# Optimization experiments

Measured on AMD Instinct MI355X. Metric: run time of the kernel, lower is better.

The kernel has to match this reference:

```python
import jax, jax.numpy as jnp
import numpy as np

B, N, K, NUM_CLASSES = 8, 4096, 20, 40


def _knn_idx(x, k):
    # x: [B, N, D] -> indices of k nearest neighbors (self excluded), [B, N, k]
    sq = jnp.sum(x * x, axis=-1)  # [B, N]
    dist = sq[:, :, None] + sq[:, None, :] - 2.0 * jnp.einsum('bnd,bmd->bnm', x, x)
    dist = jnp.where(jnp.eye(x.shape[1], dtype=bool)[None], jnp.inf, dist)
    return jax.lax.top_k(-dist, k)[1]


def _edge_conv(x, idx, params):
    # PyG EdgeConv with max aggregation: max_j MLP([x_i, x_j - x_i])
    x_j = jax.vmap(lambda xb, ib: xb[ib])(x, idx)              # [B, N, K, D]
    x_i = jnp.broadcast_to(x[:, :, None, :], x_j.shape)        # [B, N, K, D]
    h = jnp.concatenate([x_i, x_j - x_i], axis=-1)             # [B, N, K, 2D]
    for w, b in params:
        h = jax.nn.relu(h @ w + b)
    return jnp.max(h, axis=2)                                  # [B, N, out]


def setup_inputs() -> dict:
    key = jax.random.key(0)
    ks = jax.random.split(key, 12)

    def lin(k, i, o):  # torch Linear default init
        k1, k2 = jax.random.split(k)
        s = 1.0 / np.sqrt(i)
        return (jax.random.uniform(k1, (i, o), jnp.float32, -s, s),
                jax.random.uniform(k2, (o,), jnp.float32, -s, s))

    inp = {
        'pos': jax.random.normal(ks[0], (B * N, 3), jnp.float32),
        'batch': jnp.repeat(jnp.arange(B, dtype=jnp.int32), N),
    }
    names = [('m1w1', 'm1b1', 6, 64), ('m1w2', 'm1b2', 64, 64), ('m1w3', 'm1b3', 64, 64),
             ('m2w1', 'm2b1', 128, 128), ('m2w2', 'm2b2', 128, 128), ('m2w3', 'm2b3', 128, 256),
             ('lin0_w', 'lin0_b', 256, 512), ('lin1_w', 'lin1_b', 512, 256),
             ('lin2_w', 'lin2_b', 256, 256), ('lin3_w', 'lin3_b', 256, NUM_CLASSES)]
    for t, (wn, bn, i, o) in enumerate(names):
        w, b = lin(ks[t + 1], i, o)
        inp[wn] = w
        inp[bn] = b
    return inp


def reference(pos, batch, m1w1, m1b1, m1w2, m1b2, m1w3, m1b3,
              m2w1, m2b1, m2w2, m2b2, m2w3, m2b3,
              lin0_w, lin0_b, lin1_w, lin1_b, lin2_w, lin2_b, lin3_w, lin3_b):
    x = pos.reshape(B, N, 3)
    x = _edge_conv(x, _knn_idx(x, K), [(m1w1, m1b1), (m1w2, m1b2), (m1w3, m1b3)])   # [B,N,64]
    x = _edge_conv(x, _knn_idx(x, K), [(m2w1, m2b1), (m2w2, m2b2), (m2w3, m2b3)])   # [B,N,256]
    x = jax.nn.relu(x @ lin0_w + lin0_b)                                            # [B,N,512]
    x = jax.ops.segment_max(x.reshape(B * N, -1), batch, num_segments=B)            # [B,512]
    x = jax.nn.relu(x @ lin1_w + lin1_b)
    x = jax.nn.relu(x @ lin2_w + lin2_b)   # dropout is identity in eval mode
    x = x @ lin3_w + lin3_b
    return jax.nn.log_softmax(x, axis=-1)
```

## Files before the change

### kernel.cpp

```cpp
#include <hip/hip_runtime.h>

#define DEVI static __device__ __forceinline__

typedef __attribute__((ext_vector_type(4))) float f32x4;
typedef __attribute__((ext_vector_type(8))) short short8;
typedef __attribute__((ext_vector_type(4))) short short4v;
typedef __attribute__((ext_vector_type(8))) __bf16 bf16x8;

#define N_    4096
#define KNN_  20
#define NPTS  32768

DEVI unsigned short f2bf(float f){
  unsigned u = __float_as_uint(f);
  u += 0x7FFFu + ((u >> 16) & 1u);
  return (unsigned short)(u >> 16);
}
DEVI float bf2f(unsigned short s){ return __uint_as_float(((unsigned)s) << 16); }
DEVI float bf2fs(short s){ return __uint_as_float(((unsigned)(unsigned short)s) << 16); }
DEVI unsigned umin32(unsigned a, unsigned b){ return a < b ? a : b; }
DEVI unsigned umax32(unsigned a, unsigned b){ return a > b ? a : b; }

DEVI f32x4 mfma16(short8 a, short8 b, f32x4 c){
  return __builtin_amdgcn_mfma_f32_16x16x32_bf16(
      __builtin_bit_cast(bf16x8, a), __builtin_bit_cast(bf16x8, b), c, 0, 0, 0);
}

DEVI short8 lds_frag(const unsigned short* buf, int row, int k0, int strideS, int swzMask){
  return *(const short8*)(buf + row*strideS + (k0 ^ ((row & swzMask) << 3)));
}
DEVI void lds_put8(unsigned short* buf, int row, int k0, int strideS, int swzMask, short8 v){
  *(short8*)(buf + row*strideS + (k0 ^ ((row & swzMask) << 3))) = v;
}
DEVI void lds_put1(unsigned short* buf, int row, int col, int strideS, int swzMask, unsigned short v){
  buf[row*strideS + (col ^ ((row & swzMask) << 3))] = v;
}

DEVI void ins32(unsigned K, unsigned (&a)[20]){
#pragma unroll
  for (int t = 19; t >= 1; --t) a[t] = umin32(a[t], umax32(a[t-1], K));
  a[0] = umin32(a[0], K);
}
DEVI void ins64(double K, double (&a)[20]){
#pragma unroll
  for (int t = 19; t >= 1; --t) a[t] = fmin(a[t], fmax(a[t-1], K));
  a[0] = fmin(a[0], K);
}

__global__ __launch_bounds__(256) void p3_k(const float* __restrict__ pos,
    unsigned short* __restrict__ p3h, unsigned short* __restrict__ p3l, float* __restrict__ nrm3){
  int p = blockIdx.x*256 + threadIdx.x;
  if (p >= NPTS) return;
  float x = pos[(size_t)p*3], y = pos[(size_t)p*3+1], z = pos[(size_t)p*3+2];
  float v[8] = {x, y, z, 0.f, 0.f, 0.f, 0.f, 0.f};
#pragma unroll
  for (int c = 0; c < 8; ++c){
    unsigned short h = f2bf(v[c]);
    p3h[(size_t)p*8 + c] = h;
    p3l[(size_t)p*8 + c] = f2bf(v[c] - bf2f(h));
  }
  nrm3[p] = fmaf(x, x, fmaf(y, y, z*z));
}

template<int MODE>
__global__ __launch_bounds__(256) void knn_k(const unsigned short* __restrict__ Xh,
                                             const unsigned short* __restrict__ Xl,
                                             const float* __restrict__ nrm,
                                             unsigned* __restrict__ pk){
  constexpr int OBL  = MODE ? 8192  : 1024;
  constexpr int OS   = MODE ? 16384 : 2048;
  constexpr int OBUF = MODE ? 33536 : 19200;
  constexpr int OSQ  = MODE ? 39680 : 25344;
  __shared__ __align__(16) char smem[MODE ? 39936 : 25600];
  unsigned short* Bh = (unsigned short*)(smem);
  unsigned short* Bl = (unsigned short*)(smem + OBL);
  unsigned* S        = (unsigned*)(smem + OS);
  unsigned* buf      = (unsigned*)(smem + OBUF);
  float* sqj         = (float*)(smem + OSQ);
  unsigned* mD       = (unsigned*)(smem);

  const int blk = blockIdx.x;
  const int rt = blk & 63, ch = (blk >> 6) & 1, bb = blk >> 7;
  const int rowbase = rt * 64, cbase = ch * 2048;
  const size_t gb = (size_t)bb * N_;
  const int tid = threadIdx.x, lane = tid & 63, wid = tid >> 6;
  const int l15 = lane & 15, kL = (lane >> 4) << 3, r0 = (lane >> 4) << 2;

  short8 ah0 = {0,0,0,0,0,0,0,0}, ah1 = {0,0,0,0,0,0,0,0};
  short8 al0 = {0,0,0,0,0,0,0,0}, al1 = {0,0,0,0,0,0,0,0};
  const int arow = rowbase + (wid << 4) + l15;
  if (MODE == 1){
    const size_t ab = (gb + arow) * 64;
    ah0 = *(const short8*)(Xh + ab + kL);
    ah1 = *(const short8*)(Xh + ab + 32 + kL);
    al0 = *(const short8*)(Xl + ab + kL);
    al1 = *(const short8*)(Xl + ab + 32 + kL);
  } else {
    if (lane < 16){
      const size_t ab = (gb + arow) * 8;
      ah0 = *(const short8*)(Xh + ab);
      al0 = *(const short8*)(Xl + ab);
    }
  }
  float sqi[4];
#pragma unroll
  for (int r = 0; r < 4; ++r) sqi[r] = nrm[gb + rowbase + (wid << 4) + r0 + r];

  unsigned arr[20];
#pragma unroll
  for (int t = 0; t < 20; ++t) arr[t] = 0xFFFFFFFFu;
  unsigned thrP = 0xFFFFFFFFu;
  int cnt = 0;
  const int srow = tid & 63, q = tid >> 6;

  for (int c = 0; c < 32; ++c){
    __syncthreads();
    if (MODE == 1){
      for (int f = tid; f < 512; f += 256){
        int lf = f & 63, half = (f >> 6) & 1, nt = f >> 7;
        int row = nt*16 + (lf & 15);
        int col = half*32 + ((lf >> 4) << 3);
        const size_t src = (gb + cbase + c*64 + row) * 64 + col;
        *(short8*)(Bh + f*8) = *(const short8*)(Xh + src);
        *(short8*)(Bl + f*8) = *(const short8*)(Xl + src);
      }
    } else {
      if (tid < 64)       *(short8*)(Bh + tid*8)      = *(const short8*)(Xh + (gb + cbase + c*64 + tid)*8);
      else if (tid < 128) *(short8*)(Bl + (tid-64)*8) = *(const short8*)(Xl + (gb + cbase + c*64 + (tid-64))*8);
    }
    if (tid < 64) sqj[tid] = nrm[gb + cbase + c*64 + tid];
    __syncthreads();

    const bool selfTile = (cbase + c*64 == rowbase);
#pragma unroll
    for (int nt = 0; nt < 4; ++nt){
      f32x4 acc = {0.f,0.f,0.f,0.f};
      if (MODE == 1){
        const int fb = lane*8;
        short8 bh0 = *(const short8*)(Bh + (nt*2+0)*512 + fb);
        short8 bh1 = *(const short8*)(Bh + (nt*2+1)*512 + fb);
        short8 bl0 = *(const short8*)(Bl + (nt*2+0)*512 + fb);
        short8 bl1 = *(const short8*)(Bl + (nt*2+1)*512 + fb);
        acc = mfma16(ah0, bh0, acc); acc = mfma16(ah1, bh1, acc);
        acc = mfma16(ah0, bl0, acc); acc = mfma16(ah1, bl1, acc);
        acc = mfma16(al0, bh0, acc); acc = mfma16(al1, bh1, acc);
      } else {
        int br = nt*16 + l15;
        short8 bh = {0,0,0,0,0,0,0,0}, bl = {0,0,0,0,0,0,0,0};
        if (lane < 16){
          bh = *(const short8*)(Bh + br*8);
          bl = *(const short8*)(Bl + br*8);
        }
        acc = mfma16(ah0, bh, acc);
        acc = mfma16(ah0, bl, acc);
        acc = mfma16(al0, bh, acc);
      }
      int col = nt*16 + l15;
      float sj = sqj[col];
      unsigned cid = (unsigned)(c*64 + col);
#pragma unroll
      for (int r = 0; r < 4; ++r){
        int row = (wid << 4) + r0 + r;
        float dv = fmaxf(fmaf(-2.f, acc[r], sqi[r] + sj), 0.f);
        unsigned kb = (__float_as_uint(dv) & ~0x7FFu) | cid;
        if (selfTile && col == row) kb = 0x7F800000u | cid;
        S[row*67 + col] = kb;
      }
    }
    __syncthreads();

    {
      const unsigned* Sr = S + srow*67 + q*16;
#pragma unroll
      for (int u = 0; u < 16; ++u){
        unsigned kb = Sr[u];
        if (kb < thrP){
          if (cnt < 6){ buf[cnt*256 + tid] = kb; ++cnt; }
          else ins32(kb, arr);
        }
      }
      for (int t = 0; t < cnt; ++t) ins32(buf[t*256 + tid], arr);
      cnt = 0;
      thrP = arr[19];
    }
  }
  __syncthreads();
  if (q > 0){
#pragma unroll
    for (int t = 0; t < 20; ++t) mD[(srow*3 + q-1)*20 + t] = arr[t];
  }
  __syncthreads();
  if (q == 0){
    for (int qq = 0; qq < 3; ++qq)
#pragma unroll
      for (int t = 0; t < 20; ++t) ins32(mD[(srow*3 + qq)*20 + t], arr);
    const size_t gp = gb + rowbase + srow;
#pragma unroll
    for (int t = 0; t < 20; ++t) pk[((size_t)(ch*20 + t))*NPTS + gp] = arr[t];
  }
}

__global__ __launch_bounds__(256) void knn_merge_k(const unsigned* __restrict__ pk,
                                                   int* __restrict__ idx){
  const int p = blockIdx.x*256 + threadIdx.x;
  double arr[20];
#pragma unroll
  for (int t = 0; t < 20; ++t){
    unsigned k = pk[(size_t)t*NPTS + p];
    unsigned long long K = (((unsigned long long)(k & ~0x7FFu)) << 1) | (k & 0x7FFu);
    arr[t] = __builtin_bit_cast(double, K);
  }
#pragma unroll
  for (int t = 0; t < 20; ++t){
    unsigned k = pk[(size_t)(20 + t)*NPTS + p];
    unsigned long long K = (((unsigned long long)(k & ~0x7FFu)) << 1) | (2048u + (k & 0x7FFu));
    ins64(__builtin_bit_cast(double, K), arr);
  }
  int* o = idx + (size_t)p*KNN_;
#pragma unroll
  for (int t = 0; t < 20; ++t)
    o[t] = (int)(__builtin_bit_cast(unsigned long long, arr[t]) & 0xFFFu);
}

__global__ void stage_w_k(const float* __restrict__ src, unsigned short* __restrict__ dh,
                          unsigned short* __restrict__ dl, int K, int Nw, int KT, int NT){
  int tid = blockIdx.x*256 + threadIdx.x;
  if (tid >= NT*KT*64) return;
  int l = tid & 63;
  int kk = (tid >> 6) % KT;
  int nt = tid / (64*KT);
  int n = nt*16 + (l & 15);
  int kb = kk*32 + ((l >> 4) << 3);
#pragma unroll
  for (int e=0;e<8;++e){
    int k = kb + e;
    float w = (k < K) ? src[(size_t)k*Nw + n] : 0.f;
    unsigned short h = f2bf(w);
    dh[(size_t)tid*8 + e] = h;
    if (dl) dl[(size_t)tid*8 + e] = f2bf(w - bf2f(h));
  }
}

__global__ __launch_bounds__(256) void ec1_k(const float* __restrict__ pos, const int* __restrict__ idx1,
    const unsigned short* __restrict__ W1h, const unsigned short* __restrict__ W1l,
    const unsigned short* __restrict__ W2h, const unsigned short* __restrict__ W2l,
    const unsigned short* __restrict__ W3h, const unsigned short* __restrict__ W3l,
    const float* __restrict__ b1, const float* __restrict__ b2, const float* __restrict__ b3,
    unsigned short* __restrict__ x1h, unsigned short* __restrict__ x1l, float* __restrict__ nrm1){
  __shared__ __align__(16) char smem[52224];
  unsigned short* Ah  = (unsigned short*)(smem);
  unsigned short* Al  = (unsigned short*)(smem + 5120);
  unsigned short* H1h = (unsigned short*)(smem + 10240);
  unsigned short* H1l = (unsigned short*)(smem + 20480);
  unsigned short* H2h = (unsigned short*)(smem + 30720);
  unsigned short* H2l = (unsigned short*)(smem + 40960);
  unsigned* pmax = (unsigned*)(smem + 51200);
  const int p0 = blockIdx.x * 4;
  const int bb = p0 >> 12;
  const int tid = threadIdx.x, lane = tid & 63, wid = tid >> 6;
  pmax[tid] = 0u;
  if (tid < 80){
    int p = p0 + tid/20, slot = tid%20;
    int j = idx1[(size_t)p*KNN_ + slot];
    int gj = (bb << 12) + j;
    float a6[6];
    a6[0] = pos[(size_t)p*3]; a6[1] = pos[(size_t)p*3+1]; a6[2] = pos[(size_t)p*3+2];
    a6[3] = pos[(size_t)gj*3]   - a6[0];
    a6[4] = pos[(size_t)gj*3+1] - a6[1];
    a6[5] = pos[(size_t)gj*3+2] - a6[2];
#pragma unroll
    for (int q=0;q<4;++q){
      short8 vh, vl;
#pragma unroll
      for (int c=0;c<8;++c){
        int cc = q*8+c;
        float v = 0.f;
        if (cc < 6) v = a6[cc];
        unsigned short h = f2bf(v);
        vh[c] = (short)h;
        vl[c] = (short)f2bf(v - bf2f(h));
      }
      lds_put8(Ah, tid, q*8, 32, 3, vh);
      lds_put8(Al, tid, q*8, 32, 3, vl);
    }
  }
  __syncthreads();
  const int l15 = lane & 15, kL = (lane >> 4) << 3, r0 = (lane >> 4) << 2;
  {
    int nt = wid;
    short8 wh = *(const short8*)(W1h + ((size_t)nt*64 + lane)*8);
    short8 wl = *(const short8*)(W1l + ((size_t)nt*64 + lane)*8);
    float bias = b1[nt*16 + l15];
    for (int mt=0; mt<5; ++mt){
      int ar = mt*16 + l15;
      short8 ah = lds_frag(Ah, ar, kL, 32, 3);
      short8 al = lds_frag(Al, ar, kL, 32, 3);
      f32x4 acc = {0.f,0.f,0.f,0.f};
      acc = mfma16(ah, wh, acc);
      acc = mfma16(ah, wl, acc);
      acc = mfma16(al, wh, acc);
#pragma unroll
      for (int r=0;r<4;++r){
        int row = mt*16 + r0 + r;
        float v = fmaxf(acc[r] + bias, 0.f);
        unsigned short h = f2bf(v);
        lds_put1(H1h, row, nt*16+l15, 64, 7, h);
        lds_put1(H1l, row, nt*16+l15, 64, 7, f2bf(v - bf2f(h)));
      }
    }
  }
  __syncthreads();
  {
    int nt = wid;
    short8 wh0 = *(const short8*)(W2h + ((size_t)(nt*2+0)*64 + lane)*8);
    short8 wh1 = *(const short8*)(W2h + ((size_t)(nt*2+1)*64 + lane)*8);
    short8 wl0 = *(const short8*)(W2l + ((size_t)(nt*2+0)*64 + lane)*8);
    short8 wl1 = *(const short8*)(W2l + ((size_t)(nt*2+1)*64 + lane)*8);
    float bias = b2[nt*16 + l15];
    for (int mt=0; mt<5; ++mt){
      int ar = mt*16 + l15;
      short8 ah0 = lds_frag(H1h, ar, kL,      64, 7);
      short8 ah1 = lds_frag(H1h, ar, 32 + kL, 64, 7);
      short8 al0 = lds_frag(H1l, ar, kL,      64, 7);
      short8 al1 = lds_frag(H1l, ar, 32 + kL, 64, 7);
      f32x4 acc = {0.f,0.f,0.f,0.f};
      acc = mfma16(ah0, wh0, acc); acc = mfma16(ah1, wh1, acc);
      acc = mfma16(ah0, wl0, acc); acc = mfma16(ah1, wl1, acc);
      acc = mfma16(al0, wh0, acc); acc = mfma16(al1, wh1, acc);
#pragma unroll
      for (int r=0;r<4;++r){
        int row = mt*16 + r0 + r;
        float v = fmaxf(acc[r] + bias, 0.f);
        unsigned short h = f2bf(v);
        lds_put1(H2h, row, nt*16+l15, 64, 7, h);
        lds_put1(H2l, row, nt*16+l15, 64, 7, f2bf(v - bf2f(h)));
      }
    }
  }
  __syncthreads();
  {
    int nt = wid;
    short8 wh0 = *(const short8*)(W3h + ((size_t)(nt*2+0)*64 + lane)*8);
    short8 wh1 = *(const short8*)(W3h + ((size_t)(nt*2+1)*64 + lane)*8);
    short8 wl0 = *(const short8*)(W3l + ((size_t)(nt*2+0)*64 + lane)*8);
    short8 wl1 = *(const short8*)(W3l + ((size_t)(nt*2+1)*64 + lane)*8);
    float bias = b3[nt*16 + l15];
    for (int mt=0; mt<5; ++mt){
      int ar = mt*16 + l15;
      short8 ah0 = lds_frag(H2h, ar, kL,      64, 7);
      short8 ah1 = lds_frag(H2h, ar, 32 + kL, 64, 7);
      short8 al0 = lds_frag(H2l, ar, kL,      64, 7);
      short8 al1 = lds_frag(H2l, ar, 32 + kL, 64, 7);
      f32x4 acc = {0.f,0.f,0.f,0.f};
      acc = mfma16(ah0, wh0, acc); acc = mfma16(ah1, wh1, acc);
      acc = mfma16(ah0, wl0, acc); acc = mfma16(ah1, wl1, acc);
      acc = mfma16(al0, wh0, acc); acc = mfma16(al1, wh1, acc);
#pragma unroll
      for (int r=0;r<4;++r){
        int row = mt*16 + r0 + r;
        float v = fmaxf(acc[r] + bias, 0.f);
        atomicMax(&pmax[(row/20)*64 + nt*16 + l15], __float_as_uint(v));
      }
    }
  }
  __syncthreads();
  if (tid < 128){
    int p = tid >> 5, cp = tid & 31;
    int c0 = cp*2, c1 = c0 + 1;
    float m0 = __uint_as_float(pmax[p*64 + c0]);
    float m1 = __uint_as_float(pmax[p*64 + c1]);
    int gp = p0 + p;
    unsigned short h0 = f2bf(m0), h1v = f2bf(m1);
    x1h[(size_t)gp*64 + c0] = h0;
    x1h[(size_t)gp*64 + c1] = h1v;
    x1l[(size_t)gp*64 + c0] = f2bf(m0 - bf2f(h0));
    x1l[(size_t)gp*64 + c1] = f2bf(m1 - bf2f(h1v));
    float s = fmaf(m0, m0, m1*m1);
    s += __shfl_xor(s, 1, 32); s += __shfl_xor(s, 2, 32); s += __shfl_xor(s, 4, 32);
    s += __shfl_xor(s, 8, 32); s += __shfl_xor(s, 16, 32);
    if (cp == 0) nrm1[gp] = s;
  }
}

__global__ __launch_bounds__(256) void ec2_k(const unsigned short* __restrict__ x1h, const int* __restrict__ idx2,
    const unsigned short* __restrict__ V1, const unsigned short* __restrict__ V2, const unsigned short* __restrict__ V3,
    const float* __restrict__ b1, const float* __restrict__ b2, const float* __restrict__ b3,
    unsigned short* __restrict__ x2b){
  __shared__ __align__(16) char smem[81920];
  unsigned short* A  = (unsigned short*)(smem);
  unsigned short* H1 = (unsigned short*)(smem + 40960);
  const int p0 = blockIdx.x * 8, bb = p0 >> 12;
  const int tid = threadIdx.x, lane = tid & 63, wid = tid >> 6;
  const int l15 = lane & 15, r0 = (lane >> 4) << 2;

  if (tid < 160){
    int p = p0 + tid/20, slot = tid%20;
    int j = idx2[(size_t)p*KNN_ + slot];
    int gj = (bb << 12) + j;
    const unsigned short* xi = x1h + (size_t)p*64;
    const unsigned short* xj = x1h + (size_t)gj*64;
    int mt = tid >> 4, lrow = tid & 15;
#pragma unroll
    for (int q=0;q<8;++q){
      short8 vi = *(const short8*)(xi + q*8);
      short8 vj = *(const short8*)(xj + q*8);
      short8 vd;
#pragma unroll
      for (int c=0;c<8;++c) vd[c] = (short)f2bf(bf2fs(vj[c]) - bf2fs(vi[c]));
      *(short8*)(A + (((mt*4 + (q>>2))*64) + (q&3)*16 + lrow)*8) = vi;
      *(short8*)(A + (((mt*4 + 2 + (q>>2))*64) + (q&3)*16 + lrow)*8) = vd;
    }
  }
  __syncthreads();

  {
    short8 w[2][4];
#pragma unroll
    for (int ni=0;ni<2;++ni)
#pragma unroll
      for (int kk=0;kk<4;++kk)
        w[ni][kk] = *(const short8*)(V1 + ((size_t)((wid*2+ni)*4+kk)*64 + lane)*8);
    f32x4 b4[2];
    b4[0] = *(const f32x4*)(b1 + (wid*2+0)*16 + r0);
    b4[1] = *(const f32x4*)(b1 + (wid*2+1)*16 + r0);
    for (int mt=0; mt<10; ++mt){
      short8 bfr[4];
#pragma unroll
      for (int kk=0;kk<4;++kk) bfr[kk] = *(const short8*)(A + ((mt*4+kk)*64 + lane)*8);
#pragma unroll
      for (int ni=0;ni<2;++ni){
        int nt = wid*2 + ni;
        f32x4 acc = {0.f,0.f,0.f,0.f};
#pragma unroll
        for (int kk=0;kk<4;++kk) acc = mfma16(w[ni][kk], bfr[kk], acc);
        short4v v4;
#pragma unroll
        for (int r=0;r<4;++r) v4[r] = (short)f2bf(fmaxf(acc[r] + b4[ni][r], 0.f));
        int kk2 = nt >> 1, sub2 = (nt & 1)*2 + (r0 >> 3);
        *(short4v*)(H1 + ((mt*4+kk2)*64 + sub2*16 + l15)*8 + (r0 & 4)) = v4;
      }
    }
  }
  __syncthreads();
  {
    short8 w[2][4];
#pragma unroll
    for (int ni=0;ni<2;++ni)
#pragma unroll
      for (int kk=0;kk<4;++kk)
        w[ni][kk] = *(const short8*)(V2 + ((size_t)((wid*2+ni)*4+kk)*64 + lane)*8);
    f32x4 b4[2];
    b4[0] = *(const f32x4*)(b2 + (wid*2+0)*16 + r0);
    b4[1] = *(const f32x4*)(b2 + (wid*2+1)*16 + r0);
    for (int mt=0; mt<10; ++mt){
      short8 bfr[4];
#pragma unroll
      for (int kk=0;kk<4;++kk) bfr[kk] = *(const short8*)(H1 + ((mt*4+kk)*64 + lane)*8);
#pragma unroll
      for (int ni=0;ni<2;++ni){
        int nt = wid*2 + ni;
        f32x4 acc = {0.f,0.f,0.f,0.f};
#pragma unroll
        for (int kk=0;kk<4;++kk) acc = mfma16(w[ni][kk], bfr[kk], acc);
        short4v v4;
#pragma unroll
        for (int r=0;r<4;++r) v4[r] = (short)f2bf(fmaxf(acc[r] + b4[ni][r], 0.f));
        int kk2 = nt >> 1, sub2 = (nt & 1)*2 + (r0 >> 3);
        *(short4v*)(A + ((mt*4+kk2)*64 + sub2*16 + l15)*8 + (r0 & 4)) = v4;
      }
    }
  }
  __syncthreads();
  for (int g2=0; g2<2; ++g2){
    {
      short8 w[2][4];
#pragma unroll
      for (int ni=0;ni<2;++ni)
#pragma unroll
        for (int kk=0;kk<4;++kk)
          w[ni][kk] = *(const short8*)(V3 + ((size_t)((g2*8 + wid*2+ni)*4+kk)*64 + lane)*8);
      f32x4 b4[2];
      b4[0] = *(const f32x4*)(b3 + (g2*8 + wid*2+0)*16 + r0);
      b4[1] = *(const f32x4*)(b3 + (g2*8 + wid*2+1)*16 + r0);
      for (int mt=0; mt<10; ++mt){
        short8 bfr[4];
#pragma unroll
        for (int kk=0;kk<4;++kk) bfr[kk] = *(const short8*)(A + ((mt*4+kk)*64 + lane)*8);
#pragma unroll
        for (int ni=0;ni<2;++ni){
          int ntl = wid*2 + ni;
          f32x4 acc = {0.f,0.f,0.f,0.f};
#pragma unroll
          for (int kk=0;kk<4;++kk) acc = mfma16(w[ni][kk], bfr[kk], acc);
          short4v v4;
#pragma unroll
          for (int r=0;r<4;++r) v4[r] = (short)f2bf(fmaxf(acc[r] + b4[ni][r], 0.f));
          int kk2 = ntl >> 1, sub2 = (ntl & 1)*2 + (r0 >> 3);
          *(short4v*)(H1 + ((mt*4+kk2)*64 + sub2*16 + l15)*8 + (r0 & 4)) = v4;
        }
      }
    }
    __syncthreads();
    if (tid < 128){
      int p = tid >> 4, c8 = tid & 15;
      int kk = c8 >> 2, sub = c8 & 3;
      unsigned short mx[8];
#pragma unroll
      for (int e=0;e<8;++e) mx[e] = 0;
      for (int e=0;e<20;++e){
        int ee = e + p + c8; ee -= (ee >= 20) ? 20 : 0; ee -= (ee >= 20) ? 20 : 0;
        int row = p*20 + ee;
        short8 v = *(const short8*)(H1 + (((row>>4)*4 + kk)*64 + sub*16 + (row & 15))*8);
#pragma unroll
        for (int k2=0;k2<8;++k2){
          unsigned short u = (unsigned short)v[k2];
          mx[k2] = u > mx[k2] ? u : mx[k2];
        }
      }
      short8 o;
#pragma unroll
      for (int k2=0;k2<8;++k2) o[k2] = (short)mx[k2];
      *(short8*)(x2b + (size_t)(p0 + p)*256 + g2*128 + c8*8) = o;
    }
    __syncthreads();
  }
}

__global__ __launch_bounds__(256) void lin0_k(const unsigned short* __restrict__ x2b, const unsigned short* __restrict__ W0s,
                                              const float* __restrict__ b0, unsigned* __restrict__ pool){
  __shared__ __align__(16) char smem[67584];
  unsigned short* A = (unsigned short*)(smem);
  unsigned* ploc = (unsigned*)(smem + 65536);
  const int blk = blockIdx.x; const size_t row0 = (size_t)blk * 128; const int bb = blk >> 5;
  const int tid = threadIdx.x, lane = tid & 63, wid = tid >> 6;
  for (int it = tid; it < 4096; it += 256){
    int row = it >> 5, q = (it & 31) << 3;
    lds_put8(A, row, q, 256, 7, *(const short8*)(x2b + (row0 + row)*256 + q));
  }
  ploc[tid] = 0u; ploc[tid+256] = 0u;
  __syncthreads();
  const int l15 = lane & 15, kL = (lane >> 4) << 3;
  short8 af[2][8];
#pragma unroll
  for (int m=0;m<2;++m)
#pragma unroll
    for (int kk=0;kk<8;++kk)
      af[m][kk] = lds_frag(A, (wid*2+m)*16 + l15, kk*32 + kL, 256, 7);
  for (int nt=0; nt<32; ++nt){
    f32x4 a0 = {0.f,0.f,0.f,0.f}, a1 = {0.f,0.f,0.f,0.f};
#pragma unroll
    for (int kk=0;kk<8;++kk){
      short8 w = *(const short8*)(W0s + ((size_t)(nt*8+kk)*64 + lane)*8);
      a0 = mfma16(af[0][kk], w, a0);
      a1 = mfma16(af[1][kk], w, a1);
    }
    int col = nt*16 + l15;
    float m = fmaxf(fmaxf(fmaxf(a0[0],a0[1]),fmaxf(a0[2],a0[3])),
                    fmaxf(fmaxf(a1[0],a1[1]),fmaxf(a1[2],a1[3])));
    m = fmaxf(m + b0[col], 0.f);
    atomicMax(&ploc[col], __float_as_uint(m));
  }
  __syncthreads();
  atomicMax(&pool[(size_t)bb*512 + tid], ploc[tid]);
  atomicMax(&pool[(size_t)bb*512 + tid + 256], ploc[tid+256]);
}

__global__ __launch_bounds__(256) void head_k(const unsigned* __restrict__ pool,
    const float* __restrict__ w1, const float* __restrict__ bb1,
    const float* __restrict__ w2, const float* __restrict__ bb2,
    const float* __restrict__ w3, const float* __restrict__ bb3,
    float* __restrict__ out){
  __shared__ float pl[8*512];
  __shared__ float y1[8*256];
  __shared__ float y2[8*256];
  __shared__ float lg[8*40];
  const int tid = threadIdx.x;
  for (int it = tid; it < 4096; it += 256) pl[it] = __uint_as_float(pool[it]);
  __syncthreads();
  {
    float acc[8]; float bv = bb1[tid];
#pragma unroll
    for (int r=0;r<8;++r) acc[r] = bv;
    for (int k=0;k<512;++k){
      float w = w1[(size_t)k*256 + tid];
#pragma unroll
      for (int r=0;r<8;++r) acc[r] = fmaf(pl[r*512+k], w, acc[r]);
    }
#pragma unroll
    for (int r=0;r<8;++r) y1[r*256+tid] = fmaxf(acc[r], 0.f);
  }
  __syncthreads();
  {
    float acc[8]; float bv = bb2[tid];
#pragma unroll
    for (int r=0;r<8;++r) acc[r] = bv;
    for (int k=0;k<256;++k){
      float w = w2[(size_t)k*256 + tid];
#pragma unroll
      for (int r=0;r<8;++r) acc[r] = fmaf(y1[r*256+k], w, acc[r]);
    }
#pragma unroll
    for (int r=0;r<8;++r) y2[r*256+tid] = fmaxf(acc[r], 0.f);
  }
  __syncthreads();
  if (tid < 40){
    float acc[8]; float bv = bb3[tid];
#pragma unroll
    for (int r=0;r<8;++r) acc[r] = bv;
    for (int k=0;k<256;++k){
      float w = w3[(size_t)k*40 + tid];
#pragma unroll
      for (int r=0;r<8;++r) acc[r] = fmaf(y2[r*256+k], w, acc[r]);
    }
#pragma unroll
    for (int r=0;r<8;++r) lg[r*40+tid] = acc[r];
  }
  __syncthreads();
  if (tid < 8){
    float m = -__builtin_inff();
    for (int c2=0;c2<40;++c2) m = fmaxf(m, lg[tid*40+c2]);
    float s = 0.f;
    for (int c2=0;c2<40;++c2) s += expf(lg[tid*40+c2] - m);
    float L = logf(s);
    for (int c2=0;c2<40;++c2) out[tid*40+c2] = lg[tid*40+c2] - m - L;
  }
}

extern "C" void kernel_launch(void* const* d_in, const int* in_sizes, int n_in,
                              void* d_out, int out_size, void* d_ws, size_t ws_size,
                              hipStream_t stream){
  (void)in_sizes; (void)n_in; (void)out_size; (void)ws_size;
  const float* pos  = (const float*)d_in[0];
  const float* m1w1 = (const float*)d_in[2];  const float* m1b1 = (const float*)d_in[3];
  const float* m1w2 = (const float*)d_in[4];  const float* m1b2 = (const float*)d_in[5];
  const float* m1w3 = (const float*)d_in[6];  const float* m1b3 = (const float*)d_in[7];
  const float* m2w1 = (const float*)d_in[8];  const float* m2b1 = (const float*)d_in[9];
  const float* m2w2 = (const float*)d_in[10]; const float* m2b2 = (const float*)d_in[11];
  const float* m2w3 = (const float*)d_in[12]; const float* m2b3 = (const float*)d_in[13];
  const float* l0w  = (const float*)d_in[14]; const float* l0b  = (const float*)d_in[15];
  const float* l1w  = (const float*)d_in[16]; const float* l1b  = (const float*)d_in[17];
  const float* l2w  = (const float*)d_in[18]; const float* l2b  = (const float*)d_in[19];
  const float* l3w  = (const float*)d_in[20]; const float* l3b  = (const float*)d_in[21];

  char* ws = (char*)d_ws;
  size_t o = 0;
  auto alloc = [&](size_t bytes){ size_t r = o; o += (bytes + 255) & ~(size_t)255; return r; };
  size_t o_idx1 = alloc((size_t)NPTS*20*4);
  size_t o_idx2 = alloc((size_t)NPTS*20*4);
  size_t o_x1h  = alloc((size_t)NPTS*64*2);
  size_t o_x1l  = alloc((size_t)NPTS*64*2);
  size_t o_nrm  = alloc((size_t)NPTS*4);
  size_t o_x2b  = alloc((size_t)NPTS*256*2);
  size_t o_pool = alloc(8*512*4);
  size_t o_p3h  = alloc((size_t)NPTS*8*2);
  size_t o_p3l  = alloc((size_t)NPTS*8*2);
  size_t o_nrm3 = alloc((size_t)NPTS*4);
  size_t o_pk   = alloc((size_t)2*20*NPTS*4);
  size_t o_W1h = alloc(4*1*64*8*2),  o_W1l = alloc(4*1*64*8*2);
  size_t o_W2h = alloc(4*2*64*8*2),  o_W2l = alloc(4*2*64*8*2);
  size_t o_W3h = alloc(4*2*64*8*2),  o_W3l = alloc(4*2*64*8*2);
  size_t o_V1  = alloc(8*4*64*8*2);
  size_t o_V2  = alloc(8*4*64*8*2);
  size_t o_V3  = alloc(16*4*64*8*2);
  size_t o_W0  = alloc(32*8*64*8*2);

  hipMemsetAsync(ws + o_pool, 0, 8*512*4, stream);

  stage_w_k<<<1,256,0,stream>>>(m1w1, (unsigned short*)(ws+o_W1h), (unsigned short*)(ws+o_W1l), 6, 64, 1, 4);
  stage_w_k<<<2,256,0,stream>>>(m1w2, (unsigned short*)(ws+o_W2h), (unsigned short*)(ws+o_W2l), 64, 64, 2, 4);
  stage_w_k<<<2,256,0,stream>>>(m1w3, (unsigned short*)(ws+o_W3h), (unsigned short*)(ws+o_W3l), 64, 64, 2, 4);
  stage_w_k<<<8,256,0,stream>>>(m2w1, (unsigned short*)(ws+o_V1), nullptr, 128, 128, 4, 8);
  stage_w_k<<<8,256,0,stream>>>(m2w2, (unsigned short*)(ws+o_V2), nullptr, 128, 128, 4, 8);
  stage_w_k<<<16,256,0,stream>>>(m2w3, (unsigned short*)(ws+o_V3), nullptr, 128, 256, 4, 16);
  stage_w_k<<<64,256,0,stream>>>(l0w,  (unsigned short*)(ws+o_W0), nullptr, 256, 512, 8, 32);

  p3_k<<<128,256,0,stream>>>(pos, (unsigned short*)(ws+o_p3h), (unsigned short*)(ws+o_p3l), (float*)(ws+o_nrm3));

  knn_k<0><<<1024,256,0,stream>>>((const unsigned short*)(ws+o_p3h), (const unsigned short*)(ws+o_p3l),
                                  (const float*)(ws+o_nrm3), (unsigned*)(ws+o_pk));
  knn_merge_k<<<128,256,0,stream>>>((const unsigned*)(ws+o_pk), (int*)(ws+o_idx1));

  ec1_k<<<8192,256,0,stream>>>(pos, (const int*)(ws+o_idx1),
      (const unsigned short*)(ws+o_W1h), (const unsigned short*)(ws+o_W1l),
      (const unsigned short*)(ws+o_W2h), (const unsigned short*)(ws+o_W2l),
      (const unsigned short*)(ws+o_W3h), (const unsigned short*)(ws+o_W3l),
      m1b1, m1b2, m1b3,
      (unsigned short*)(ws+o_x1h), (unsigned short*)(ws+o_x1l), (float*)(ws+o_nrm));

  knn_k<1><<<1024,256,0,stream>>>((const unsigned short*)(ws+o_x1h), (const unsigned short*)(ws+o_x1l),
                                  (const float*)(ws+o_nrm), (unsigned*)(ws+o_pk));
  knn_merge_k<<<128,256,0,stream>>>((const unsigned*)(ws+o_pk), (int*)(ws+o_idx2));

  ec2_k<<<4096,256,0,stream>>>((const unsigned short*)(ws+o_x1h), (const int*)(ws+o_idx2),
      (const unsigned short*)(ws+o_V1), (const unsigned short*)(ws+o_V2), (const unsigned short*)(ws+o_V3),
      m2b1, m2b2, m2b3, (unsigned short*)(ws+o_x2b));

  lin0_k<<<256,256,0,stream>>>((const unsigned short*)(ws+o_x2b), (const unsigned short*)(ws+o_W0),
                               l0b, (unsigned*)(ws+o_pool));

  head_k<<<1,256,0,stream>>>((const unsigned*)(ws+o_pool), l1w, l1b, l2w, l2b, l3w, l3b, (float*)d_out);
}
```

Measured before the change: 715.0 us.

## Prefetch next kNN column tile into registers and share per-row thresholds

The kNN tile kernel now issues global loads for the next 64-column tile into registers before the selection phase, then writes them to shared memory after the barrier, overlapping load latency with top-k insertion. The four threads handling a row now share a pruning threshold through an LDS atomicMin, so each thread filters against the tightest of the four partial top-20 lists. The score matrix stride changes from 67 to 68 so rows can be read as 16-byte vectors. This adds registers and an LDS atomic per tile, and the stride change may bring back bank conflicts on the score writes.

```diff
diff --git a/kernel.cpp b/kernel.cpp
--- a/kernel.cpp
+++ b/kernel.cpp
@@ -5,6 +5,7 @@
 typedef __attribute__((ext_vector_type(4))) float f32x4;
 typedef __attribute__((ext_vector_type(8))) short short8;
 typedef __attribute__((ext_vector_type(4))) short short4v;
+typedef __attribute__((ext_vector_type(4))) unsigned uint4v;
 typedef __attribute__((ext_vector_type(8))) __bf16 bf16x8;
 
 #define N_    4096
@@ -69,13 +70,15 @@
                                              unsigned* __restrict__ pk){
   constexpr int OBL  = MODE ? 8192  : 1024;
   constexpr int OS   = MODE ? 16384 : 2048;
-  constexpr int OBUF = MODE ? 33536 : 19200;
-  constexpr int OSQ  = MODE ? 39680 : 25344;
-  __shared__ __align__(16) char smem[MODE ? 39936 : 25600];
+  constexpr int OBUF = OS + 17408;
+  constexpr int OTHR = OBUF + 6144;
+  constexpr int OSQ  = OTHR + 256;
+  __shared__ __align__(16) char smem[OSQ + 256];
   unsigned short* Bh = (unsigned short*)(smem);
   unsigned short* Bl = (unsigned short*)(smem + OBL);
   unsigned* S        = (unsigned*)(smem + OS);
   unsigned* buf      = (unsigned*)(smem + OBUF);
+  unsigned* rowThr   = (unsigned*)(smem + OTHR);
   float* sqj         = (float*)(smem + OSQ);
   unsigned* mD       = (unsigned*)(smem);
 
@@ -85,6 +88,8 @@
   const size_t gb = (size_t)bb * N_;
   const int tid = threadIdx.x, lane = tid & 63, wid = tid >> 6;
   const int l15 = lane & 15, kL = (lane >> 4) << 3, r0 = (lane >> 4) << 2;
+
+  if (tid < 64) rowThr[tid] = 0xFFFFFFFFu;
 
   short8 ah0 = {0,0,0,0,0,0,0,0}, ah1 = {0,0,0,0,0,0,0,0};
   short8 al0 = {0,0,0,0,0,0,0,0}, al1 = {0,0,0,0,0,0,0,0};
@@ -109,28 +114,26 @@
   unsigned arr[20];
 #pragma unroll
   for (int t = 0; t < 20; ++t) arr[t] = 0xFFFFFFFFu;
-  unsigned thrP = 0xFFFFFFFFu;
   int cnt = 0;
   const int srow = tid & 63, q = tid >> 6;
 
+  if (MODE == 1){
+    for (int f = tid; f < 512; f += 256){
+      int lf = f & 63, half = (f >> 6) & 1, nt = f >> 7;
+      int row = nt*16 + (lf & 15);
+      int col = half*32 + ((lf >> 4) << 3);
+      const size_t src = (gb + cbase + row) * 64 + col;
+      *(short8*)(Bh + f*8) = *(const short8*)(Xh + src);
+      *(short8*)(Bl + f*8) = *(const short8*)(Xl + src);
+    }
+  } else {
+    if (tid < 64)       *(short8*)(Bh + tid*8)      = *(const short8*)(Xh + (gb + cbase + tid)*8);
+    else if (tid < 128) *(short8*)(Bl + (tid-64)*8) = *(const short8*)(Xl + (gb + cbase + (tid-64))*8);
+  }
+  if (tid < 64) sqj[tid] = nrm[gb + cbase + tid];
+  __syncthreads();
+
   for (int c = 0; c < 32; ++c){
-    __syncthreads();
-    if (MODE == 1){
-      for (int f = tid; f < 512; f += 256){
-        int lf = f & 63, half = (f >> 6) & 1, nt = f >> 7;
-        int row = nt*16 + (lf & 15);
-        int col = half*32 + ((lf >> 4) << 3);
-        const size_t src = (gb + cbase + c*64 + row) * 64 + col;
-        *(short8*)(Bh + f*8) = *(const short8*)(Xh + src);
-        *(short8*)(Bl + f*8) = *(const short8*)(Xl + src);
-      }
-    } else {
-      if (tid < 64)       *(short8*)(Bh + tid*8)      = *(const short8*)(Xh + (gb + cbase + c*64 + tid)*8);
-      else if (tid < 128) *(short8*)(Bl + (tid-64)*8) = *(const short8*)(Xl + (gb + cbase + c*64 + (tid-64))*8);
-    }
-    if (tid < 64) sqj[tid] = nrm[gb + cbase + c*64 + tid];
-    __syncthreads();
-
     const bool selfTile = (cbase + c*64 == rowbase);
 #pragma unroll
     for (int nt = 0; nt < 4; ++nt){
@@ -164,27 +167,65 @@
         float dv = fmaxf(fmaf(-2.f, acc[r], sqi[r] + sj), 0.f);
         unsigned kb = (__float_as_uint(dv) & ~0x7FFu) | cid;
         if (selfTile && col == row) kb = 0x7F800000u | cid;
-        S[row*67 + col] = kb;
-      }
+        S[row*68 + col] = kb;
+      }
+    }
+    short8 nh0 = {0,0,0,0,0,0,0,0}, nh1 = {0,0,0,0,0,0,0,0};
+    short8 nl0 = {0,0,0,0,0,0,0,0}, nl1 = {0,0,0,0,0,0,0,0};
+    float nsq = 0.f;
+    const bool more = (c + 1 < 32);
+    if (more){
+      if (MODE == 1){
+#pragma unroll
+        for (int ff = 0; ff < 2; ++ff){
+          int f = tid + ff*256;
+          int lf = f & 63, half = (f >> 6) & 1, nt = f >> 7;
+          int row = nt*16 + (lf & 15);
+          int col = half*32 + ((lf >> 4) << 3);
+          const size_t src = (gb + cbase + (c+1)*64 + row) * 64 + col;
+          if (ff == 0){ nh0 = *(const short8*)(Xh + src); nl0 = *(const short8*)(Xl + src); }
+          else        { nh1 = *(const short8*)(Xh + src); nl1 = *(const short8*)(Xl + src); }
+        }
+      } else {
+        if (tid < 64)       nh0 = *(const short8*)(Xh + (gb + cbase + (c+1)*64 + tid)*8);
+        else if (tid < 128) nl0 = *(const short8*)(Xl + (gb + cbase + (c+1)*64 + (tid-64))*8);
+      }
+      if (tid < 64) nsq = nrm[gb + cbase + (c+1)*64 + tid];
     }
     __syncthreads();
-
+    if (more){
+      if (MODE == 1){
+        *(short8*)(Bh + tid*8)       = nh0;
+        *(short8*)(Bh + (tid+256)*8) = nh1;
+        *(short8*)(Bl + tid*8)       = nl0;
+        *(short8*)(Bl + (tid+256)*8) = nl1;
+      } else {
+        if (tid < 64)       *(short8*)(Bh + tid*8)      = nh0;
+        else if (tid < 128) *(short8*)(Bl + (tid-64)*8) = nl0;
+      }
+      if (tid < 64) sqj[tid] = nsq;
+    }
     {
-      const unsigned* Sr = S + srow*67 + q*16;
-#pragma unroll
-      for (int u = 0; u < 16; ++u){
-        unsigned kb = Sr[u];
-        if (kb < thrP){
-          if (cnt < 6){ buf[cnt*256 + tid] = kb; ++cnt; }
-          else ins32(kb, arr);
+      unsigned thrP = rowThr[srow];
+      const uint4v* Sr4 = (const uint4v*)(S + srow*68 + q*16);
+#pragma unroll
+      for (int u4 = 0; u4 < 4; ++u4){
+        uint4v v = Sr4[u4];
+#pragma unroll
+        for (int e = 0; e < 4; ++e){
+          unsigned kb = v[e];
+          if (kb < thrP){
+            if (cnt < 6){ buf[cnt*256 + tid] = kb; ++cnt; }
+            else ins32(kb, arr);
+          }
         }
       }
       for (int t = 0; t < cnt; ++t) ins32(buf[t*256 + tid], arr);
       cnt = 0;
-      thrP = arr[19];
-    }
-  }
-  __syncthreads();
+      atomicMin(&rowThr[srow], arr[19]);
+    }
+    __syncthreads();
+  }
   if (q > 0){
 #pragma unroll
     for (int t = 0; t < 20; ++t) mD[(srow*3 + q-1)*20 + t] = arr[t];
```

Result: faster. 655.4 us (-8.3%).
